# Kernel tuning notes

Hardware: AMD Instinct MI355X
Metric: run time of the kernel (lower is better)

Reference implementation:

```python
import jax, jax.numpy as jnp
import numpy as np

C, SHOT, D = 64, 16, 320
LN_EPS = 1e-5


def setup_inputs() -> dict:
    key = jax.random.key(0)
    ks = jax.random.split(key, 20)
    s = 0.05
    inp = {
        "input_x_mean": jax.random.normal(ks[0], (C, D), jnp.float32),
        "input_x": jax.random.normal(ks[1], (C * SHOT, D), jnp.float32),
        # embedding_same / embedding_diff Linear(D, D)
        "W_same": jax.random.normal(ks[2], (D, D), jnp.float32) * s,
        "b_same": jnp.zeros((D,), jnp.float32),
        "W_diff": jax.random.normal(ks[3], (D, D), jnp.float32) * s,
        "b_diff": jnp.zeros((D,), jnp.float32),
        # 1-head MultiHeadAttention(d_model=d_k=d_v=D)
        "Wq": jax.random.normal(ks[4], (D, D), jnp.float32) * s,
        "bq": jnp.zeros((D,), jnp.float32),
        "Wk": jax.random.normal(ks[5], (D, D), jnp.float32) * s,
        "bk": jnp.zeros((D,), jnp.float32),
        "Wv": jax.random.normal(ks[6], (D, D), jnp.float32) * s,
        "bv": jnp.zeros((D,), jnp.float32),
        "Wfc": jax.random.normal(ks[7], (D, D), jnp.float32) * s,
        "bfc": jnp.zeros((D,), jnp.float32),
        "ln_g": jnp.ones((D,), jnp.float32),
        "ln_b": jnp.zeros((D,), jnp.float32),
        # output Linear(D, 1)
        "Wout": jax.random.normal(ks[8], (D, 1), jnp.float32) * s,
        "bout": jnp.zeros((1,), jnp.float32),
    }
    return inp


def _mha(q, k, v, Wq, bq, Wk, bk, Wv, bv, Wfc, bfc, ln_g, ln_b):
    # Standard 1-head attention: proj -> scaled softmax attn -> fc -> residual + LayerNorm
    residual = q
    temp = jnp.sqrt(jnp.asarray(q.shape[-1], q.dtype))
    qp = q @ Wq + bq
    kp = k @ Wk + bk
    vp = v @ Wv + bv
    attn = jax.nn.softmax(jnp.einsum('bld,bmd->blm', qp, kp) / temp, axis=-1)
    out = jnp.einsum('blm,bmd->bld', attn, vp)
    out = out @ Wfc + bfc
    out = out + residual
    mu = out.mean(-1, keepdims=True)
    var = ((out - mu) ** 2).mean(-1, keepdims=True)
    return ln_g * (out - mu) * jax.lax.rsqrt(var + LN_EPS) + ln_b


def reference(input_x_mean, input_x, W_same, b_same, W_diff, b_diff,
              Wq, bq, Wk, bk, Wv, bv, Wfc, bfc, ln_g, ln_b, Wout, bout):
    c, d = input_x_mean.shape
    shot = input_x.shape[0] // c
    x = input_x.reshape(c, shot, d)

    # ---- Difference_Estimator ----
    same_diff = x - input_x_mean[:, None, :]                     # (C, shot, D)
    cls = np.arange(c)
    other = np.stack([np.concatenate([cls[:i], cls[i + 1:]]) for i in range(c)])  # (C, C-1)
    idx = (other[:, :, None] * shot + np.arange(shot)[None, None, :]).reshape(c, (c - 1) * shot)
    diff_diff = input_x_mean[:, None, :] - input_x[idx]          # (C, (C-1)*shot, D)

    # ---- Mean_Aggregator (one odefunc evaluation; state = input_x_mean) ----
    ps = (same_diff @ W_same + b_same) - input_x_mean[:, None, :]
    pd = (diff_diff @ W_diff + b_diff) - input_x_mean[:, None, :]
    ts = _mha(ps, ps, ps, Wq, bq, Wk, bk, Wv, bv, Wfc, bfc, ln_g, ln_b)
    td = _mha(pd, pd, pd, Wq, bq, Wk, bk, Wv, bv, Wfc, bfc, ln_g, ln_b)
    sm_s = jax.nn.softmax(ts @ Wout + bout, axis=1)              # (C, shot, 1)
    sm_d = jax.nn.softmax(td @ Wout + bout, axis=1)              # (C, (C-1)*shot, 1)
    weighted = jnp.concatenate([sm_s * ps, sm_d * pd], axis=1)   # (C, C*shot, D)
    return weighted.mean(axis=1)                                 # (C, D)
```

## Files before the change

kernel.cpp:

```cpp
#include <hip/hip_runtime.h>

#define CC   64
#define SHOT 16
#define DD   320
#define ND   1008
#define MS   (CC * SHOT)
#define MD   (CC * ND)
#define MT   (MD + MS)
#define LN_EPS 1e-5f

typedef __attribute__((ext_vector_type(8)))  short short8;
typedef __attribute__((ext_vector_type(4)))  float floatx4;
typedef __attribute__((ext_vector_type(4)))  int i32x4;

__device__ __forceinline__ unsigned short f2b(float f) {
  union { float f; unsigned int u; } v; v.f = f;
  unsigned int r = v.u + 0x7FFFu + ((v.u >> 16) & 1u);
  return (unsigned short)(r >> 16);
}
__device__ __forceinline__ float b2f(unsigned short b) {
  union { unsigned int u; float f; } v; v.u = ((unsigned int)b) << 16; return v.f;
}
__device__ __forceinline__ unsigned int pk2(float a, float b) {
  return (unsigned int)f2b(a) | ((unsigned int)f2b(b) << 16);
}
__device__ __forceinline__ void gl_lds16(const void* g, void* l) {
  __builtin_amdgcn_global_load_lds(
      (const __attribute__((address_space(1))) unsigned int*)g,
      (__attribute__((address_space(3))) unsigned int*)l, 16, 0, 0);
}
__device__ __forceinline__ floatx4 mfma16(short8 a, short8 b, floatx4 c) {
  return __builtin_amdgcn_mfma_f32_16x16x32_bf16(a, b, c, 0, 0, 0);
}
#define BARRIER_VM()  do { asm volatile("s_waitcnt vmcnt(0) lgkmcnt(0)" ::: "memory"); \
                           __builtin_amdgcn_s_barrier(); \
                           __builtin_amdgcn_sched_barrier(0); } while (0)

__global__ __launch_bounds__(256, 2) void gemm_mfma(
    const unsigned short* __restrict__ A,
    const float* __restrict__ Xg, const float* __restrict__ Xmean,
    const int mode,
    const unsigned short* __restrict__ BtDiff,
    const unsigned short* __restrict__ BtSame,
    const float* __restrict__ biasDiff, const float* __restrict__ biasSame,
    unsigned short* __restrict__ OutB,
    const unsigned short* __restrict__ ResB)
{
  __shared__ __align__(16) unsigned short As[2][128 * 64];
  __shared__ __align__(16) unsigned short Bs[2][64 * 64];
  const int t  = threadIdx.x;
  const int m0 = blockIdx.x * 128;
  const int n0 = blockIdx.y * 64;
  const int wid = t >> 6, lane = t & 63;
  const int wm = wid >> 1, wn = wid & 1;
  const int l15 = lane & 15, lg = lane >> 4;

  const bool isDiff = (m0 < MD);
  const unsigned short* Bt = (mode == 3 && !isDiff) ? BtSame : BtDiff;
  const float* bias = (mode == 3 && !isDiff) ? biasSame : biasDiff;

  const int ra = t >> 1, kh = t & 1;
  const float* aptr = nullptr; const float* mptr = nullptr;
  float sa = 1.f;
  if (mode == 3) {
    const int am = m0 + ra;
    if (isDiff) {
      const int c = am / ND, j = am - c * ND;
      const int oi = j >> 4, s = j & 15;
      const int oc = (oi < c) ? oi : oi + 1;
      aptr = Xg + (size_t)(oc * SHOT + s) * DD;
      mptr = Xmean + (size_t)c * DD;
      sa = -1.f;
    } else {
      const int ls = am - MD;
      aptr = Xg + (size_t)ls * DD;
      mptr = Xmean + (size_t)(ls >> 4) * DD;
      sa = 1.f;
    }
  }

  floatx4 acc[4][2];
  #pragma unroll
  for (int i = 0; i < 4; ++i)
    #pragma unroll
    for (int j = 0; j < 2; ++j) acc[i][j] = (floatx4){0.f, 0.f, 0.f, 0.f};

  auto stage = [&](int ks, int bufi) {
    const int k0 = ks * 64;
    #pragma unroll
    for (int it = 0; it < 2; ++it) {
      const int L = it * 256 + t;
      const int r = L >> 3, cs = L & 7;
      const int cl = cs ^ (r & 7);
      gl_lds16(Bt + (size_t)(n0 + r) * DD + k0 + cl * 8, &Bs[bufi][0] + L * 8);
    }
    if (mode == 0) {
      #pragma unroll
      for (int it = 0; it < 4; ++it) {
        const int L = it * 256 + t;
        const int r = L >> 3, cs = L & 7;
        const int cl = cs ^ (r & 7);
        gl_lds16(A + (size_t)(m0 + r) * DD + k0 + cl * 8, &As[bufi][0] + L * 8);
      }
    } else {
      const int kb2 = k0 + kh * 32;
      #pragma unroll
      for (int i = 0; i < 4; ++i) {
        const float4 x0  = *(const float4*)(aptr + kb2 + i * 8);
        const float4 x1  = *(const float4*)(aptr + kb2 + i * 8 + 4);
        const float4 mv0 = *(const float4*)(mptr + kb2 + i * 8);
        const float4 mv1 = *(const float4*)(mptr + kb2 + i * 8 + 4);
        i32x4 w;
        w[0] = (int)pk2(sa * (x0.x - mv0.x), sa * (x0.y - mv0.y));
        w[1] = (int)pk2(sa * (x0.z - mv0.z), sa * (x0.w - mv0.w));
        w[2] = (int)pk2(sa * (x1.x - mv1.x), sa * (x1.y - mv1.y));
        w[3] = (int)pk2(sa * (x1.z - mv1.z), sa * (x1.w - mv1.w));
        const int c  = kh * 4 + i;
        const int cw = c ^ (ra & 7);
        *(i32x4*)((char*)&As[bufi][0] + ra * 128 + cw * 16) = w;
      }
    }
  };

  auto compute = [&](int bufi) {
    #pragma unroll
    for (int kc = 0; kc < 2; ++kc) {
      short8 af[4], bf[2];
      #pragma unroll
      for (int mt = 0; mt < 4; ++mt) {
        const int row = wm * 64 + mt * 16 + l15;
        const int cs  = (kc * 4 + lg) ^ (row & 7);
        af[mt] = *(const short8*)((const char*)&As[bufi][0] + row * 128 + cs * 16);
      }
      #pragma unroll
      for (int nt = 0; nt < 2; ++nt) {
        const int row = wn * 32 + nt * 16 + l15;
        const int cs  = (kc * 4 + lg) ^ (row & 7);
        bf[nt] = *(const short8*)((const char*)&Bs[bufi][0] + row * 128 + cs * 16);
      }
      #pragma unroll
      for (int mt = 0; mt < 4; ++mt)
        #pragma unroll
        for (int nt = 0; nt < 2; ++nt)
          acc[mt][nt] = mfma16(af[mt], bf[nt], acc[mt][nt]);
    }
  };

  stage(0, 0);
  BARRIER_VM();
  for (int ks = 0; ks < 5; ++ks) {
    if (ks + 1 < 5) stage(ks + 1, (ks + 1) & 1);
    compute(ks & 1);
    BARRIER_VM();
  }

  #pragma unroll
  for (int nt = 0; nt < 2; ++nt) {
    const int n = n0 + wn * 32 + nt * 16 + l15;
    const float bb = bias[n];
    #pragma unroll
    for (int mt = 0; mt < 4; ++mt) {
      #pragma unroll
      for (int r = 0; r < 4; ++r) {
        const int m = m0 + wm * 64 + mt * 16 + lg * 4 + r;
        float v = acc[mt][nt][r] + bb;
        if (mode == 3) {
          const int cm = isDiff ? (m / ND) : ((m - MD) >> 4);
          v -= Xmean[(size_t)cm * DD + n];
        }
        if (ResB) v += b2f(ResB[(size_t)m * DD + n]);
        OutB[(size_t)m * DD + n] = f2b(v);
      }
    }
  }
}

__global__ __launch_bounds__(256, 2) void attn16(
    const unsigned short* __restrict__ Qg, const unsigned short* __restrict__ Pk,
    const unsigned short* __restrict__ Pt, unsigned short* __restrict__ Ob,
    const int qRows,
    const int kPitch,
    const int vtPitch,
    const int nKT, const int validKV, const int bpc, const int qTiles)
{
  __shared__ __align__(16) char smem[64 * 656];
  const int t = threadIdx.x;
  const int wid = t >> 6, lane = t & 63;
  const int l15 = lane & 15, lg = lane >> 4;

  int bx = blockIdx.x;
  const int nwg = gridDim.x;
  if ((nwg & 7) == 0) bx = (bx & 7) * (nwg >> 3) + (bx >> 3);
  const int cls  = bx / bpc;
  const int blkq = bx - cls * bpc;
  const int qt0 = blkq * 4 + wid;
  const bool wValid = qt0 < qTiles;
  const int qt = wValid ? qt0 : qTiles - 1;

  short8 qf[10];
  {
    const unsigned short* qrow = Qg + ((size_t)cls * qRows + qt * 16 + l15) * DD;
    #pragma unroll
    for (int kc = 0; kc < 10; ++kc) qf[kc] = *(const short8*)(qrow + kc * 32 + lg * 8);
  }

  floatx4 o[20];
  #pragma unroll
  for (int i = 0; i < 20; ++i) o[i] = (floatx4){0.f, 0.f, 0.f, 0.f};
  float mrun = -1e30f, lsum = 0.f;
  const float scale = 0.05590169943749474f;

  for (int kt = 0; kt < nKT; ++kt) {
    __syncthreads();
    #pragma unroll
    for (int it = 0; it < 5; ++it) {
      const int L = it * 256 + t;
      const int r = L / 40, c = L - (L / 40) * 40;
      const int cl = (c & ~7) | ((c & 7) ^ (r & 7));
      gl_lds16(Pk + ((size_t)cls * kPitch + kt * 32 + r) * DD + cl * 8, smem + L * 16);
    }
    #pragma unroll
    for (int it = 0; it < 5; ++it) {
      const int L = it * 256 + t;
      const int d = L >> 2, c = L & 3;
      const int cl = c ^ ((d >> 1) & 3);
      gl_lds16(Pt + ((size_t)cls * DD + d) * vtPitch + kt * 32 + cl * 8,
               smem + 20480 + L * 16);
    }
    __syncthreads();

    floatx4 st0 = (floatx4){0.f,0.f,0.f,0.f}, st1 = (floatx4){0.f,0.f,0.f,0.f};
    __builtin_amdgcn_s_setprio(1);
    #pragma unroll
    for (int kc = 0; kc < 10; ++kc) {
      const int c = kc * 4 + lg;
      const int cl = (c & ~7) | ((c & 7) ^ (l15 & 7));
      const short8 k0f = *(const short8*)(smem + l15 * 640 + cl * 16);
      const short8 k1f = *(const short8*)(smem + (16 + l15) * 640 + cl * 16);
      st0 = mfma16(k0f, qf[kc], st0);
      st1 = mfma16(k1f, qf[kc], st1);
    }
    __builtin_amdgcn_s_setprio(0);

    float s[8];
    #pragma unroll
    for (int r = 0; r < 4; ++r) { s[r] = st0[r] * scale; s[4 + r] = st1[r] * scale; }
    const int kvb = kt * 32 + lg * 4;
    #pragma unroll
    for (int r = 0; r < 4; ++r) {
      if (kvb + r      >= validKV) s[r]     = -1e30f;
      if (kvb + 16 + r >= validKV) s[4 + r] = -1e30f;
    }
    float mt_ = s[0];
    #pragma unroll
    for (int i = 1; i < 8; ++i) mt_ = fmaxf(mt_, s[i]);
    mt_ = fmaxf(mt_, __shfl_xor(mt_, 16));
    mt_ = fmaxf(mt_, __shfl_xor(mt_, 32));
    const float newm = fmaxf(mrun, mt_);
    if (__any(newm > mrun)) {
      const float alpha = __expf(mrun - newm);
      lsum *= alpha;
      #pragma unroll
      for (int i = 0; i < 20; ++i) {
        o[i][0] *= alpha; o[i][1] *= alpha; o[i][2] *= alpha; o[i][3] *= alpha;
      }
      mrun = newm;
    }
    float p[8]; float rs = 0.f;
    #pragma unroll
    for (int i = 0; i < 8; ++i) { p[i] = __expf(s[i] - mrun); rs += p[i]; }
    rs += __shfl_xor(rs, 16);
    rs += __shfl_xor(rs, 32);
    lsum += rs;

    const unsigned int pk00 = pk2(p[0], p[1]), pk01 = pk2(p[2], p[3]);
    const unsigned int pk10 = pk2(p[4], p[5]), pk11 = pk2(p[6], p[7]);
    const int src0 = l15 + ((lane >> 4) & 1) * 32;
    const int src1 = src0 + 16;
    const int y0 = __shfl((int)pk00, src0), y1 = __shfl((int)pk01, src0);
    const int y2 = __shfl((int)pk00, src1), y3 = __shfl((int)pk01, src1);
    const int z0 = __shfl((int)pk10, src0), z1 = __shfl((int)pk11, src0);
    const int z2 = __shfl((int)pk10, src1), z3 = __shfl((int)pk11, src1);
    const bool hi = lane >= 32;
    union { i32x4 w; short8 v; } pf;
    pf.w[0] = hi ? z0 : y0; pf.w[1] = hi ? z1 : y1;
    pf.w[2] = hi ? z2 : y2; pf.w[3] = hi ? z3 : y3;

    const int vswz = (l15 >> 1) & 3;
    __builtin_amdgcn_s_setprio(1);
    #pragma unroll
    for (int dt = 0; dt < 20; ++dt) {
      const int d = dt * 16 + l15;
      const short8 a = *(const short8*)(smem + 20480 + d * 64 + ((lg ^ vswz) << 4));
      o[dt] = mfma16(a, pf.v, o[dt]);
    }
    __builtin_amdgcn_s_setprio(0);
  }

  const float invl = 1.f / lsum;
  __syncthreads();
  char* ep = smem + wid * 10496;
  #pragma unroll
  for (int dt = 0; dt < 20; ++dt) {
    const unsigned int w0 = pk2(o[dt][0] * invl, o[dt][1] * invl);
    const unsigned int w1 = pk2(o[dt][2] * invl, o[dt][3] * invl);
    *(unsigned int*)(ep + l15 * 656 + (dt * 16 + lg * 4) * 2)     = w0;
    *(unsigned int*)(ep + l15 * 656 + (dt * 16 + lg * 4 + 2) * 2) = w1;
  }
  __syncthreads();
  if (wValid) {
    #pragma unroll
    for (int it = 0; it < 10; ++it) {
      const int flat = it * 64 + lane;
      const int q = flat / 40, c = flat - (flat / 40) * 40;
      const i32x4 v = *(const i32x4*)(ep + q * 656 + c * 16);
      *(i32x4*)(Ob + ((size_t)cls * qRows + qt * 16 + q) * DD + c * 8) = v;
    }
  }
}

__global__ __launch_bounds__(256) void transpose_p(
    const unsigned short* __restrict__ P, unsigned short* __restrict__ PtG,
    const int rowsP, const int vtPitch, const int kvTilesPerCls)
{
  __shared__ __align__(16) unsigned short Ls[64 * 72];
  const int t = threadIdx.x;
  const int cls = blockIdx.x / kvTilesPerCls;
  const int kvt = blockIdx.x - cls * kvTilesPerCls;
  const int dt = blockIdx.y;
  #pragma unroll
  for (int i = 0; i < 2; ++i) {
    const int flat = t + i * 256;
    const int r = flat >> 3, c = flat & 7;
    const int kv = kvt * 64 + r;
    i32x4 v = {0, 0, 0, 0};
    if (kv < rowsP)
      v = *(const i32x4*)(P + ((size_t)cls * rowsP + kv) * DD + dt * 64 + c * 8);
    *(i32x4*)(&Ls[r * 72 + c * 8]) = v;
  }
  __syncthreads();
  #pragma unroll
  for (int i = 0; i < 2; ++i) {
    const int flat = t + i * 256;
    const int r2 = flat >> 3, c2 = flat & 7;
    if (kvt * 64 + c2 * 8 < vtPitch) {
      union { unsigned short e[8]; i32x4 v; } u;
      #pragma unroll
      for (int jj = 0; jj < 8; ++jj) u.e[jj] = Ls[(c2 * 8 + jj) * 72 + r2];
      *(i32x4*)(PtG + ((size_t)cls * DD + dt * 64 + r2) * vtPitch + kvt * 64 + c2 * 8) = u.v;
    }
  }
}

__global__ __launch_bounds__(256) void wprep(
    const float* __restrict__ Wsame, const float* __restrict__ Wdiff,
    const float* __restrict__ Wk, const float* __restrict__ Wq,
    const float* __restrict__ Wfc, const float* __restrict__ Wv,
    unsigned short* __restrict__ BtS, unsigned short* __restrict__ BtD,
    unsigned short* __restrict__ BtG, unsigned short* __restrict__ BtVF)
{
  __shared__ float Ls[64 * 68];
  const int t = threadIdx.x;
  const int z = blockIdx.z;
  if (z < 2) {
    const float* W = z ? Wdiff : Wsame;
    unsigned short* Wt = z ? BtD : BtS;
    const int k0 = blockIdx.x * 64, n0 = blockIdx.y * 64;
    #pragma unroll
    for (int i = 0; i < 4; ++i) {
      const int flat = t + i * 256;
      const int r = flat >> 4, c = (flat & 15) * 4;
      *(float4*)&Ls[r * 68 + c] = *(const float4*)(W + (size_t)(k0 + r) * DD + n0 + c);
    }
    __syncthreads();
    #pragma unroll
    for (int j = 0; j < 2; ++j) {
      const int flat = t + j * 256;
      const int r2 = flat >> 3, c2 = flat & 7;
      union { unsigned short e[8]; i32x4 v; } u;
      #pragma unroll
      for (int jj = 0; jj < 8; ++jj) u.e[jj] = f2b(Ls[(c2 * 8 + jj) * 68 + r2]);
      *(i32x4*)(Wt + (size_t)(n0 + r2) * DD + k0 + c2 * 8) = u.v;
    }
  } else {
    const int trL = (z == 3);
    const float* L = trL ? Wfc : Wk;
    const float* R = trL ? Wv : Wq;
    unsigned short* Bt = trL ? BtVF : BtG;
    float* Lsm = Ls;
    float* Rsm = Ls + 16 * 68;
    const int n0 = blockIdx.x * 64, k0 = blockIdx.y * 64;
    const int tn4 = (t & 15) * 4, tk4 = (t >> 4) * 4;
    float acc[4][4] = {};
    for (int ms = 0; ms < DD; ms += 16) {
      const int lr = t >> 4, lc = (t & 15);
      #pragma unroll
      for (int i = 0; i < 4; ++i) {
        const int nn = lc * 4 + i;
        Lsm[lr * 68 + nn] = trL ? L[(size_t)(ms + lr) * DD + n0 + nn]
                                : L[(size_t)(n0 + nn) * DD + ms + lr];
        Rsm[lr * 68 + nn] = R[(size_t)(k0 + nn) * DD + ms + lr];
      }
      __syncthreads();
      #pragma unroll
      for (int mm = 0; mm < 16; ++mm) {
        float la[4], rb[4];
        #pragma unroll
        for (int i = 0; i < 4; ++i) { la[i] = Lsm[mm * 68 + tn4 + i]; rb[i] = Rsm[mm * 68 + tk4 + i]; }
        #pragma unroll
        for (int i = 0; i < 4; ++i)
          #pragma unroll
          for (int j = 0; j < 4; ++j) acc[i][j] += la[i] * rb[j];
      }
      __syncthreads();
    }
    #pragma unroll
    for (int i = 0; i < 4; ++i)
      #pragma unroll
      for (int j = 0; j < 4; ++j)
        Bt[(size_t)(n0 + tn4 + i) * DD + k0 + tk4 + j] = f2b(acc[i][j]);
  }
}

__global__ __launch_bounds__(640) void wbias(
    const float* __restrict__ Wk, const float* __restrict__ bq,
    const float* __restrict__ Wfc, const float* __restrict__ bv,
    const float* __restrict__ bfc, float* __restrict__ v, float* __restrict__ bvf)
{
  const int t = threadIdx.x;
  if (t < DD) {
    float a = 0.f;
    for (int m = 0; m < DD; ++m) a += Wk[(size_t)t * DD + m] * bq[m];
    v[t] = a;
  } else if (t < 2 * DD) {
    const int n = t - DD;
    float a = 0.f;
    for (int m = 0; m < DD; ++m) a += Wfc[(size_t)m * DD + n] * bv[m];
    bvf[n] = a + bfc[n];
  }
}

__global__ __launch_bounds__(256) void ln_logit(
    const unsigned short* __restrict__ X, const float* __restrict__ gam,
    const float* __restrict__ bet, const float* __restrict__ Wout,
    const float* __restrict__ bout, float* __restrict__ logits, const int M)
{
  const int row = blockIdx.x * 4 + (threadIdx.x >> 6);
  if (row >= M) return;
  const int lane = threadIdx.x & 63;
  const unsigned short* x = X + (size_t)row * DD;
  float v[5]; float s = 0.f;
  #pragma unroll
  for (int i = 0; i < 5; ++i) { v[i] = b2f(x[lane + 64 * i]); s += v[i]; }
  #pragma unroll
  for (int off = 32; off; off >>= 1) s += __shfl_xor(s, off);
  const float mu = s * (1.f / DD);
  float q = 0.f;
  #pragma unroll
  for (int i = 0; i < 5; ++i) { const float d = v[i] - mu; q += d * d; }
  #pragma unroll
  for (int off = 32; off; off >>= 1) q += __shfl_xor(q, off);
  const float inv = rsqrtf(q * (1.f / DD) + LN_EPS);
  float lg = 0.f;
  #pragma unroll
  for (int i = 0; i < 5; ++i) {
    const int k = lane + 64 * i;
    lg += (gam[k] * (v[i] - mu) * inv + bet[k]) * Wout[k];
  }
  #pragma unroll
  for (int off = 32; off; off >>= 1) lg += __shfl_xor(lg, off);
  if (lane == 0) logits[row] = lg + bout[0];
}

__global__ __launch_bounds__(320) void final_reduce(
    const float* __restrict__ logits_s, const float* __restrict__ logits_d,
    const unsigned short* __restrict__ Ps, const unsigned short* __restrict__ Pd,
    float* __restrict__ out)
{
  const int c = blockIdx.x;
  const int t = threadIdx.x;
  __shared__ float w[16 + ND];
  __shared__ float red[5];
  if (t < 16) w[t] = logits_s[c * 16 + t];
  for (int j = t; j < ND; j += 320) w[16 + j] = logits_d[c * ND + j];
  __syncthreads();
  if (t == 0) {
    float mx = w[0];
    #pragma unroll
    for (int i = 1; i < 16; ++i) mx = fmaxf(mx, w[i]);
    float ssum = 0.f;
    #pragma unroll
    for (int i = 0; i < 16; ++i) { const float e = __expf(w[i] - mx); w[i] = e; ssum += e; }
    const float inv = 1.f / ssum;
    #pragma unroll
    for (int i = 0; i < 16; ++i) w[i] *= inv;
  }
  float lm = -1e30f;
  for (int j = t; j < ND; j += 320) lm = fmaxf(lm, w[16 + j]);
  #pragma unroll
  for (int off = 32; off; off >>= 1) lm = fmaxf(lm, __shfl_xor(lm, off));
  if ((t & 63) == 0) red[t >> 6] = lm;
  __syncthreads();
  const float mx = fmaxf(fmaxf(fmaxf(red[0], red[1]), fmaxf(red[2], red[3])), red[4]);
  float ls = 0.f;
  for (int j = t; j < ND; j += 320) { const float e = __expf(w[16 + j] - mx); w[16 + j] = e; ls += e; }
  #pragma unroll
  for (int off = 32; off; off >>= 1) ls += __shfl_xor(ls, off);
  __syncthreads();
  if ((t & 63) == 0) red[t >> 6] = ls;
  __syncthreads();
  const float inv = 1.f / (red[0] + red[1] + red[2] + red[3] + red[4]);
  for (int j = t; j < ND; j += 320) w[16 + j] *= inv;
  __syncthreads();
  float acc = 0.f;
  const unsigned short* Psc = Ps + (size_t)c * SHOT * DD + t;
  const unsigned short* Pdc = Pd + (size_t)c * ND * DD + t;
  #pragma unroll 4
  for (int i = 0; i < 16; ++i) acc += w[i] * b2f(Psc[(size_t)i * DD]);
  for (int j = 0; j < ND; ++j) acc += w[16 + j] * b2f(Pdc[(size_t)j * DD]);
  out[c * DD + t] = acc * (1.f / 1024.f);
}

extern "C" void kernel_launch(void* const* d_in, const int* in_sizes, int n_in,
                              void* d_out, int out_size, void* d_ws, size_t ws_size,
                              hipStream_t stream)
{
  const float* xmean = (const float*)d_in[0];
  const float* x     = (const float*)d_in[1];
  const float* Wsame = (const float*)d_in[2];
  const float* bsame = (const float*)d_in[3];
  const float* Wdiff = (const float*)d_in[4];
  const float* bdiff = (const float*)d_in[5];
  const float* Wq    = (const float*)d_in[6];
  const float* bq    = (const float*)d_in[7];
  const float* Wk    = (const float*)d_in[8];
  const float* bk    = (const float*)d_in[9];   (void)bk;
  const float* Wv    = (const float*)d_in[10];
  const float* bv    = (const float*)d_in[11];
  const float* Wfc   = (const float*)d_in[12];
  const float* bfc   = (const float*)d_in[13];
  const float* lng   = (const float*)d_in[14];
  const float* lnb   = (const float*)d_in[15];
  const float* Wout  = (const float*)d_in[16];
  const float* boutp = (const float*)d_in[17];
  float* outp = (float*)d_out;

  char* base = (char*)d_ws;
  size_t off = 0;
  auto alloc = [&](size_t bytes) { char* p = base + off; off += (bytes + 255) & ~(size_t)255; return p; };

  const size_t WB = (size_t)DD * DD * 2;
  unsigned short* BtS  = (unsigned short*)alloc(WB);
  unsigned short* BtD  = (unsigned short*)alloc(WB);
  unsigned short* BtG  = (unsigned short*)alloc(WB);
  unsigned short* BtVF = (unsigned short*)alloc(WB);
  float* vbias = (float*)alloc(DD * 4);
  float* bvf   = (float*)alloc(DD * 4);
  unsigned short* P_b  = (unsigned short*)alloc((size_t)MT * DD * 2);
  unsigned short* Qg_b = (unsigned short*)alloc((size_t)MT * DD * 2);
  unsigned short* O_b  = (unsigned short*)alloc((size_t)MT * DD * 2);
  unsigned short* PtD  = (unsigned short*)alloc((size_t)CC * DD * 1024 * 2);
  unsigned short* PtS  = (unsigned short*)alloc((size_t)CC * DD * 32 * 2);
  float* logits = (float*)alloc((size_t)MT * 4);

  const dim3 blk(256);
  wprep<<<dim3(5, 5, 4), blk, 0, stream>>>(Wsame, Wdiff, Wk, Wq, Wfc, Wv,
                                           BtS, BtD, BtG, BtVF);
  wbias<<<dim3(1), dim3(640), 0, stream>>>(Wk, bq, Wfc, bv, bfc, vbias, bvf);

  const dim3 gAll(MT / 128, 5);
  gemm_mfma<<<gAll, blk, 0, stream>>>(nullptr, x, xmean, 3, BtD, BtS,
                                      bdiff, bsame, P_b, nullptr);
  transpose_p<<<dim3(CC * 16, 5), blk, 0, stream>>>(P_b, PtD, ND, 1024, 16);
  transpose_p<<<dim3(CC, 5), blk, 0, stream>>>(P_b + (size_t)MD * DD, PtS, 16, 32, 1);
  gemm_mfma<<<gAll, blk, 0, stream>>>(P_b, nullptr, nullptr, 0, BtG, nullptr,
                                      vbias, nullptr, Qg_b, nullptr);
  attn16<<<dim3(CC * 16), blk, 0, stream>>>(Qg_b, P_b, PtD, O_b,
                                            ND, ND, 1024, 32, ND, 16, 63);
  attn16<<<dim3(CC), blk, 0, stream>>>(Qg_b + (size_t)MD * DD, P_b + (size_t)MD * DD,
                                       PtS, O_b + (size_t)MD * DD,
                                       16, 16, 32, 1, 16, 1, 1);
  gemm_mfma<<<gAll, blk, 0, stream>>>(O_b, nullptr, nullptr, 0, BtVF, nullptr,
                                      bvf, nullptr, Qg_b, P_b);
  ln_logit<<<dim3(MT / 4), blk, 0, stream>>>(Qg_b, lng, lnb, Wout, boutp, logits, MT);
  final_reduce<<<dim3(CC), dim3(320), 0, stream>>>(logits + MD, logits,
                                                   P_b + (size_t)MD * DD, P_b, outp);
}
```

Measured before the change: 488.2 us.

## Fold Q·K weight product into P GEMM, fuse LayerNorm-logit into FC epilogue

The Q·Wk-style projection is precomposed with the embedding weights (Wdiff/Wsame) and the mean term, so one z-split GEMM writes both P and Qg straight from the fp32 inputs instead of a second GEMM reading P. The FC GEMM epilogue now produces per-row partial sums (sum, sum of squares, u·x), and LayerNorm plus the output projection collapse into a tiny logits kernel, removing the bf16 write and reread of the FC output. The diff and same attention launches and transposes are merged, and online-softmax rescaling is skipped unless the max grows by more than 8. Risks include extra weight-prep work, lower precision from composing weights, and E[x²]−mu² variance cancellation.

```diff
diff --git a/kernel.cpp b/kernel.cpp
--- a/kernel.cpp
+++ b/kernel.cpp
@@ -36,33 +36,35 @@
                            __builtin_amdgcn_s_barrier(); \
                            __builtin_amdgcn_sched_barrier(0); } while (0)
 
-__global__ __launch_bounds__(256, 2) void gemm_mfma(
-    const unsigned short* __restrict__ A,
+__global__ __launch_bounds__(256, 2) void gemm_p_qg(
     const float* __restrict__ Xg, const float* __restrict__ Xmean,
-    const int mode,
-    const unsigned short* __restrict__ BtDiff,
-    const unsigned short* __restrict__ BtSame,
-    const float* __restrict__ biasDiff, const float* __restrict__ biasSame,
-    unsigned short* __restrict__ OutB,
-    const unsigned short* __restrict__ ResB)
+    const unsigned short* __restrict__ BtD, const unsigned short* __restrict__ BtS,
+    const unsigned short* __restrict__ BtDG, const unsigned short* __restrict__ BtSG,
+    const float* __restrict__ bdiff, const float* __restrict__ bsame,
+    const float* __restrict__ bqg, const float* __restrict__ bsg,
+    const float* __restrict__ Mg,
+    unsigned short* __restrict__ P_b, unsigned short* __restrict__ Qg_b)
 {
   __shared__ __align__(16) unsigned short As[2][128 * 64];
   __shared__ __align__(16) unsigned short Bs[2][64 * 64];
   const int t  = threadIdx.x;
   const int m0 = blockIdx.x * 128;
   const int n0 = blockIdx.y * 64;
+  const int z  = blockIdx.z;
   const int wid = t >> 6, lane = t & 63;
   const int wm = wid >> 1, wn = wid & 1;
   const int l15 = lane & 15, lg = lane >> 4;
 
   const bool isDiff = (m0 < MD);
-  const unsigned short* Bt = (mode == 3 && !isDiff) ? BtSame : BtDiff;
-  const float* bias = (mode == 3 && !isDiff) ? biasSame : biasDiff;
+  const unsigned short* Bt = z ? (isDiff ? BtDG : BtSG) : (isDiff ? BtD : BtS);
+  const float* bias = z ? (isDiff ? bqg : bsg) : (isDiff ? bdiff : bsame);
+  const float* mean = z ? Mg : Xmean;
+  unsigned short* OutB = z ? Qg_b : P_b;
 
   const int ra = t >> 1, kh = t & 1;
-  const float* aptr = nullptr; const float* mptr = nullptr;
-  float sa = 1.f;
-  if (mode == 3) {
+  const float* aptr; const float* mptr;
+  float sa;
+  {
     const int am = m0 + ra;
     if (isDiff) {
       const int c = am / ND, j = am - c * ND;
@@ -94,31 +96,21 @@
       const int cl = cs ^ (r & 7);
       gl_lds16(Bt + (size_t)(n0 + r) * DD + k0 + cl * 8, &Bs[bufi][0] + L * 8);
     }
-    if (mode == 0) {
-      #pragma unroll
-      for (int it = 0; it < 4; ++it) {
-        const int L = it * 256 + t;
-        const int r = L >> 3, cs = L & 7;
-        const int cl = cs ^ (r & 7);
-        gl_lds16(A + (size_t)(m0 + r) * DD + k0 + cl * 8, &As[bufi][0] + L * 8);
-      }
-    } else {
-      const int kb2 = k0 + kh * 32;
-      #pragma unroll
-      for (int i = 0; i < 4; ++i) {
-        const float4 x0  = *(const float4*)(aptr + kb2 + i * 8);
-        const float4 x1  = *(const float4*)(aptr + kb2 + i * 8 + 4);
-        const float4 mv0 = *(const float4*)(mptr + kb2 + i * 8);
-        const float4 mv1 = *(const float4*)(mptr + kb2 + i * 8 + 4);
-        i32x4 w;
-        w[0] = (int)pk2(sa * (x0.x - mv0.x), sa * (x0.y - mv0.y));
-        w[1] = (int)pk2(sa * (x0.z - mv0.z), sa * (x0.w - mv0.w));
-        w[2] = (int)pk2(sa * (x1.x - mv1.x), sa * (x1.y - mv1.y));
-        w[3] = (int)pk2(sa * (x1.z - mv1.z), sa * (x1.w - mv1.w));
-        const int c  = kh * 4 + i;
-        const int cw = c ^ (ra & 7);
-        *(i32x4*)((char*)&As[bufi][0] + ra * 128 + cw * 16) = w;
-      }
+    const int kb2 = k0 + kh * 32;
+    #pragma unroll
+    for (int i = 0; i < 4; ++i) {
+      const float4 x0  = *(const float4*)(aptr + kb2 + i * 8);
+      const float4 x1  = *(const float4*)(aptr + kb2 + i * 8 + 4);
+      const float4 mv0 = *(const float4*)(mptr + kb2 + i * 8);
+      const float4 mv1 = *(const float4*)(mptr + kb2 + i * 8 + 4);
+      i32x4 w;
+      w[0] = (int)pk2(sa * (x0.x - mv0.x), sa * (x0.y - mv0.y));
+      w[1] = (int)pk2(sa * (x0.z - mv0.z), sa * (x0.w - mv0.w));
+      w[2] = (int)pk2(sa * (x1.x - mv1.x), sa * (x1.y - mv1.y));
+      w[3] = (int)pk2(sa * (x1.z - mv1.z), sa * (x1.w - mv1.w));
+      const int c  = kh * 4 + i;
+      const int cw = c ^ (ra & 7);
+      *(i32x4*)((char*)&As[bufi][0] + ra * 128 + cw * 16) = w;
     }
   };
 
@@ -163,25 +155,124 @@
       #pragma unroll
       for (int r = 0; r < 4; ++r) {
         const int m = m0 + wm * 64 + mt * 16 + lg * 4 + r;
-        float v = acc[mt][nt][r] + bb;
-        if (mode == 3) {
-          const int cm = isDiff ? (m / ND) : ((m - MD) >> 4);
-          v -= Xmean[(size_t)cm * DD + n];
-        }
-        if (ResB) v += b2f(ResB[(size_t)m * DD + n]);
+        const int cm = isDiff ? (m / ND) : ((m - MD) >> 4);
+        const float v = acc[mt][nt][r] + bb - mean[(size_t)cm * DD + n];
         OutB[(size_t)m * DD + n] = f2b(v);
       }
     }
   }
 }
 
+__global__ __launch_bounds__(256, 2) void gemm_fc(
+    const unsigned short* __restrict__ A,
+    const unsigned short* __restrict__ Bt,
+    const float* __restrict__ bvf,
+    const unsigned short* __restrict__ ResB,
+    const float* __restrict__ u,
+    float* __restrict__ part)
+{
+  __shared__ __align__(16) unsigned short As[2][128 * 64];
+  __shared__ __align__(16) unsigned short Bs[2][64 * 64];
+  const int t  = threadIdx.x;
+  const int m0 = blockIdx.x * 128;
+  const int n0 = blockIdx.y * 64;
+  const int wid = t >> 6, lane = t & 63;
+  const int wm = wid >> 1, wn = wid & 1;
+  const int l15 = lane & 15, lg = lane >> 4;
+
+  floatx4 acc[4][2];
+  #pragma unroll
+  for (int i = 0; i < 4; ++i)
+    #pragma unroll
+    for (int j = 0; j < 2; ++j) acc[i][j] = (floatx4){0.f, 0.f, 0.f, 0.f};
+
+  auto stage = [&](int ks, int bufi) {
+    const int k0 = ks * 64;
+    #pragma unroll
+    for (int it = 0; it < 2; ++it) {
+      const int L = it * 256 + t;
+      const int r = L >> 3, cs = L & 7;
+      const int cl = cs ^ (r & 7);
+      gl_lds16(Bt + (size_t)(n0 + r) * DD + k0 + cl * 8, &Bs[bufi][0] + L * 8);
+    }
+    #pragma unroll
+    for (int it = 0; it < 4; ++it) {
+      const int L = it * 256 + t;
+      const int r = L >> 3, cs = L & 7;
+      const int cl = cs ^ (r & 7);
+      gl_lds16(A + (size_t)(m0 + r) * DD + k0 + cl * 8, &As[bufi][0] + L * 8);
+    }
+  };
+
+  auto compute = [&](int bufi) {
+    #pragma unroll
+    for (int kc = 0; kc < 2; ++kc) {
+      short8 af[4], bf[2];
+      #pragma unroll
+      for (int mt = 0; mt < 4; ++mt) {
+        const int row = wm * 64 + mt * 16 + l15;
+        const int cs  = (kc * 4 + lg) ^ (row & 7);
+        af[mt] = *(const short8*)((const char*)&As[bufi][0] + row * 128 + cs * 16);
+      }
+      #pragma unroll
+      for (int nt = 0; nt < 2; ++nt) {
+        const int row = wn * 32 + nt * 16 + l15;
+        const int cs  = (kc * 4 + lg) ^ (row & 7);
+        bf[nt] = *(const short8*)((const char*)&Bs[bufi][0] + row * 128 + cs * 16);
+      }
+      #pragma unroll
+      for (int mt = 0; mt < 4; ++mt)
+        #pragma unroll
+        for (int nt = 0; nt < 2; ++nt)
+          acc[mt][nt] = mfma16(af[mt], bf[nt], acc[mt][nt]);
+    }
+  };
+
+  stage(0, 0);
+  BARRIER_VM();
+  for (int ks = 0; ks < 5; ++ks) {
+    if (ks + 1 < 5) stage(ks + 1, (ks + 1) & 1);
+    compute(ks & 1);
+    BARRIER_VM();
+  }
+
+  const int slot = blockIdx.y * 2 + wn;
+  #pragma unroll
+  for (int mt = 0; mt < 4; ++mt) {
+    float ps0[4] = {0.f,0.f,0.f,0.f}, ps1[4] = {0.f,0.f,0.f,0.f}, ps2[4] = {0.f,0.f,0.f,0.f};
+    #pragma unroll
+    for (int nt = 0; nt < 2; ++nt) {
+      const int n = n0 + wn * 32 + nt * 16 + l15;
+      const float bb = bvf[n];
+      const float un = u[n];
+      #pragma unroll
+      for (int r = 0; r < 4; ++r) {
+        const int m = m0 + wm * 64 + mt * 16 + lg * 4 + r;
+        const float v = acc[mt][nt][r] + bb + b2f(ResB[(size_t)m * DD + n]);
+        ps0[r] += v; ps1[r] += v * v; ps2[r] += un * v;
+      }
+    }
+    #pragma unroll
+    for (int r = 0; r < 4; ++r) {
+      #pragma unroll
+      for (int mk = 1; mk < 16; mk <<= 1) {
+        ps0[r] += __shfl_xor(ps0[r], mk);
+        ps1[r] += __shfl_xor(ps1[r], mk);
+        ps2[r] += __shfl_xor(ps2[r], mk);
+      }
+      if (l15 == 0) {
+        const int m = m0 + wm * 64 + mt * 16 + lg * 4 + r;
+        float* pp = part + ((size_t)m * 10 + slot) * 3;
+        pp[0] = ps0[r]; pp[1] = ps1[r]; pp[2] = ps2[r];
+      }
+    }
+  }
+}
+
 __global__ __launch_bounds__(256, 2) void attn16(
-    const unsigned short* __restrict__ Qg, const unsigned short* __restrict__ Pk,
-    const unsigned short* __restrict__ Pt, unsigned short* __restrict__ Ob,
-    const int qRows,
-    const int kPitch,
-    const int vtPitch,
-    const int nKT, const int validKV, const int bpc, const int qTiles)
+    const unsigned short* __restrict__ Qall, const unsigned short* __restrict__ Pall,
+    const unsigned short* __restrict__ PtD, const unsigned short* __restrict__ PtS,
+    unsigned short* __restrict__ Oall)
 {
   __shared__ __align__(16) char smem[64 * 656];
   const int t = threadIdx.x;
@@ -190,9 +281,20 @@
 
   int bx = blockIdx.x;
   const int nwg = gridDim.x;
-  if ((nwg & 7) == 0) bx = (bx & 7) * (nwg >> 3) + (bx >> 3);
-  const int cls  = bx / bpc;
-  const int blkq = bx - cls * bpc;
+  bx = (bx & 7) * (nwg >> 3) + (bx >> 3);
+
+  const unsigned short *Qg, *Pk, *Pt; unsigned short* Ob;
+  int cls, blkq, qRows, kPitch, vtPitch, nKT, validKV, qTiles;
+  if (bx < 1024) {
+    cls = bx >> 4; blkq = bx & 15;
+    Qg = Qall; Pk = Pall; Pt = PtD; Ob = Oall;
+    qRows = ND; kPitch = ND; vtPitch = 1024; nKT = 32; validKV = ND; qTiles = 63;
+  } else {
+    cls = bx - 1024; blkq = 0;
+    Qg = Qall + (size_t)MD * DD; Pk = Pall + (size_t)MD * DD;
+    Pt = PtS; Ob = Oall + (size_t)MD * DD;
+    qRows = 16; kPitch = 16; vtPitch = 32; nKT = 1; validKV = 16; qTiles = 1;
+  }
   const int qt0 = blkq * 4 + wid;
   const bool wValid = qt0 < qTiles;
   const int qt = wValid ? qt0 : qTiles - 1;
@@ -256,8 +358,8 @@
     for (int i = 1; i < 8; ++i) mt_ = fmaxf(mt_, s[i]);
     mt_ = fmaxf(mt_, __shfl_xor(mt_, 16));
     mt_ = fmaxf(mt_, __shfl_xor(mt_, 32));
-    const float newm = fmaxf(mrun, mt_);
-    if (__any(newm > mrun)) {
+    if (!__all(mt_ - mrun <= 8.0f)) {
+      const float newm = fmaxf(mrun, mt_);
       const float alpha = __expf(mrun - newm);
       lsum *= alpha;
       #pragma unroll
@@ -319,14 +421,19 @@
   }
 }
 
-__global__ __launch_bounds__(256) void transpose_p(
-    const unsigned short* __restrict__ P, unsigned short* __restrict__ PtG,
-    const int rowsP, const int vtPitch, const int kvTilesPerCls)
+__global__ __launch_bounds__(256) void transpose_pm(
+    const unsigned short* __restrict__ Pall,
+    unsigned short* __restrict__ PtD, unsigned short* __restrict__ PtS)
 {
   __shared__ __align__(16) unsigned short Ls[64 * 72];
   const int t = threadIdx.x;
-  const int cls = blockIdx.x / kvTilesPerCls;
-  const int kvt = blockIdx.x - cls * kvTilesPerCls;
+  const int bx = blockIdx.x;
+  const unsigned short* P; unsigned short* PtG;
+  int cls, kvt, rowsP, vtPitch;
+  if (bx < 1024) { cls = bx >> 4; kvt = bx & 15; P = Pall; PtG = PtD;
+                   rowsP = ND; vtPitch = 1024; }
+  else { cls = bx - 1024; kvt = 0; P = Pall + (size_t)MD * DD; PtG = PtS;
+         rowsP = 16; vtPitch = 32; }
   const int dt = blockIdx.y;
   #pragma unroll
   for (int i = 0; i < 2; ++i) {
@@ -357,7 +464,7 @@
     const float* __restrict__ Wk, const float* __restrict__ Wq,
     const float* __restrict__ Wfc, const float* __restrict__ Wv,
     unsigned short* __restrict__ BtS, unsigned short* __restrict__ BtD,
-    unsigned short* __restrict__ BtG, unsigned short* __restrict__ BtVF)
+    float* __restrict__ GfT, unsigned short* __restrict__ BtVF)
 {
   __shared__ float Ls[64 * 68];
   const int t = threadIdx.x;
@@ -386,7 +493,6 @@
     const int trL = (z == 3);
     const float* L = trL ? Wfc : Wk;
     const float* R = trL ? Wv : Wq;
-    unsigned short* Bt = trL ? BtVF : BtG;
     float* Lsm = Ls;
     float* Rsm = Ls + 16 * 68;
     const int n0 = blockIdx.x * 64, k0 = blockIdx.y * 64;
@@ -414,18 +520,103 @@
       }
       __syncthreads();
     }
+    if (z == 2) {
+      #pragma unroll
+      for (int i = 0; i < 4; ++i)
+        #pragma unroll
+        for (int j = 0; j < 4; ++j)
+          GfT[(size_t)(n0 + tn4 + i) * DD + k0 + tk4 + j] = acc[i][j];
+    } else {
+      #pragma unroll
+      for (int i = 0; i < 4; ++i)
+        #pragma unroll
+        for (int j = 0; j < 4; ++j)
+          BtVF[(size_t)(n0 + tn4 + i) * DD + k0 + tk4 + j] = f2b(acc[i][j]);
+    }
+  }
+}
+
+__global__ __launch_bounds__(256) void wprep2(
+    const float* __restrict__ GfT,
+    const float* __restrict__ Wdiff, const float* __restrict__ Wsame,
+    const float* __restrict__ Xmean,
+    const float* __restrict__ bdiff, const float* __restrict__ bsame,
+    const float* __restrict__ vbias,
+    unsigned short* __restrict__ BtDG, unsigned short* __restrict__ BtSG,
+    float* __restrict__ Mg, float* __restrict__ bqg, float* __restrict__ bsg)
+{
+  __shared__ float Ls[2 * 16 * 68];
+  const int t = threadIdx.x;
+  const int z = blockIdx.z;
+  if (z < 2) {
+    const float* R = z ? Wsame : Wdiff;
+    unsigned short* Bt = z ? BtSG : BtDG;
+    float* Lsm = Ls;
+    float* Rsm = Ls + 16 * 68;
+    const int n0 = blockIdx.x * 64, k0 = blockIdx.y * 64;
+    const int tn4 = (t & 15) * 4, tk4 = (t >> 4) * 4;
+    float acc[4][4] = {};
+    for (int ms = 0; ms < DD; ms += 16) {
+      const int lr = t >> 4, lc = (t & 15);
+      #pragma unroll
+      for (int i = 0; i < 4; ++i) {
+        const int nn = lc * 4 + i;
+        Lsm[lr * 68 + nn] = GfT[(size_t)(n0 + nn) * DD + ms + lr];
+        Rsm[lr * 68 + nn] = R[(size_t)(k0 + nn) * DD + ms + lr];
+      }
+      __syncthreads();
+      #pragma unroll
+      for (int mm = 0; mm < 16; ++mm) {
+        float la[4], rb[4];
+        #pragma unroll
+        for (int i = 0; i < 4; ++i) { la[i] = Lsm[mm * 68 + tn4 + i]; rb[i] = Rsm[mm * 68 + tk4 + i]; }
+        #pragma unroll
+        for (int i = 0; i < 4; ++i)
+          #pragma unroll
+          for (int j = 0; j < 4; ++j) acc[i][j] += la[i] * rb[j];
+      }
+      __syncthreads();
+    }
     #pragma unroll
     for (int i = 0; i < 4; ++i)
       #pragma unroll
       for (int j = 0; j < 4; ++j)
         Bt[(size_t)(n0 + tn4 + i) * DD + k0 + tk4 + j] = f2b(acc[i][j]);
-  }
-}
-
-__global__ __launch_bounds__(640) void wbias(
+  } else {
+    const int n0 = blockIdx.y * 64;
+    if (blockIdx.x == 0) {
+      for (int idx = t; idx < 64 * 64; idx += 256) {
+        const int c = idx >> 6, nn = n0 + (idx & 63);
+        float a = 0.f;
+        for (int k = 0; k < DD; ++k) a += Xmean[c * DD + k] * GfT[(size_t)nn * DD + k];
+        Mg[c * DD + nn] = a;
+      }
+    } else if (blockIdx.x == 1) {
+      if (t < 64) {
+        const int nn = n0 + t;
+        float a = 0.f;
+        for (int k = 0; k < DD; ++k) a += bdiff[k] * GfT[(size_t)nn * DD + k];
+        bqg[nn] = a + vbias[nn];
+      }
+    } else if (blockIdx.x == 2) {
+      if (t < 64) {
+        const int nn = n0 + t;
+        float a = 0.f;
+        for (int k = 0; k < DD; ++k) a += bsame[k] * GfT[(size_t)nn * DD + k];
+        bsg[nn] = a + vbias[nn];
+      }
+    }
+  }
+}
+
+__global__ __launch_bounds__(960) void wbias(
     const float* __restrict__ Wk, const float* __restrict__ bq,
     const float* __restrict__ Wfc, const float* __restrict__ bv,
-    const float* __restrict__ bfc, float* __restrict__ v, float* __restrict__ bvf)
+    const float* __restrict__ bfc,
+    const float* __restrict__ lng, const float* __restrict__ lnb,
+    const float* __restrict__ Wout, const float* __restrict__ bout,
+    float* __restrict__ v, float* __restrict__ bvf,
+    float* __restrict__ u, float* __restrict__ scal)
 {
   const int t = threadIdx.x;
   if (t < DD) {
@@ -437,39 +628,30 @@
     float a = 0.f;
     for (int m = 0; m < DD; ++m) a += Wfc[(size_t)m * DD + n] * bv[m];
     bvf[n] = a + bfc[n];
-  }
-}
-
-__global__ __launch_bounds__(256) void ln_logit(
-    const unsigned short* __restrict__ X, const float* __restrict__ gam,
-    const float* __restrict__ bet, const float* __restrict__ Wout,
-    const float* __restrict__ bout, float* __restrict__ logits, const int M)
-{
-  const int row = blockIdx.x * 4 + (threadIdx.x >> 6);
-  if (row >= M) return;
-  const int lane = threadIdx.x & 63;
-  const unsigned short* x = X + (size_t)row * DD;
-  float v[5]; float s = 0.f;
-  #pragma unroll
-  for (int i = 0; i < 5; ++i) { v[i] = b2f(x[lane + 64 * i]); s += v[i]; }
-  #pragma unroll
-  for (int off = 32; off; off >>= 1) s += __shfl_xor(s, off);
-  const float mu = s * (1.f / DD);
-  float q = 0.f;
-  #pragma unroll
-  for (int i = 0; i < 5; ++i) { const float d = v[i] - mu; q += d * d; }
-  #pragma unroll
-  for (int off = 32; off; off >>= 1) q += __shfl_xor(q, off);
-  const float inv = rsqrtf(q * (1.f / DD) + LN_EPS);
-  float lg = 0.f;
-  #pragma unroll
-  for (int i = 0; i < 5; ++i) {
-    const int k = lane + 64 * i;
-    lg += (gam[k] * (v[i] - mu) * inv + bet[k]) * Wout[k];
-  }
-  #pragma unroll
-  for (int off = 32; off; off >>= 1) lg += __shfl_xor(lg, off);
-  if (lane == 0) logits[row] = lg + bout[0];
+  } else if (t < 3 * DD) {
+    const int n = t - 2 * DD;
+    u[n] = lng[n] * Wout[n];
+    if (n == 0) {
+      float su = 0.f, b0 = 0.f;
+      for (int k = 0; k < DD; ++k) { su += lng[k] * Wout[k]; b0 += lnb[k] * Wout[k]; }
+      scal[0] = su; scal[1] = b0 + bout[0];
+    }
+  }
+}
+
+__global__ __launch_bounds__(256) void logits_k(
+    const float* __restrict__ part, const float* __restrict__ scal,
+    float* __restrict__ logits)
+{
+  const int m = blockIdx.x * 256 + threadIdx.x;
+  const float* pp = part + (size_t)m * 30;
+  float sF = 0.f, sF2 = 0.f, sUF = 0.f;
+  #pragma unroll
+  for (int s = 0; s < 10; ++s) { sF += pp[s * 3]; sF2 += pp[s * 3 + 1]; sUF += pp[s * 3 + 2]; }
+  const float mu  = sF * (1.f / DD);
+  const float var = sF2 * (1.f / DD) - mu * mu;
+  const float inv = rsqrtf(var + LN_EPS);
+  logits[m] = inv * (sUF - mu * scal[0]) + scal[1];
 }
 
 __global__ __launch_bounds__(320) void final_reduce(
@@ -552,37 +734,38 @@
   const size_t WB = (size_t)DD * DD * 2;
   unsigned short* BtS  = (unsigned short*)alloc(WB);
   unsigned short* BtD  = (unsigned short*)alloc(WB);
-  unsigned short* BtG  = (unsigned short*)alloc(WB);
+  unsigned short* BtDG = (unsigned short*)alloc(WB);
+  unsigned short* BtSG = (unsigned short*)alloc(WB);
   unsigned short* BtVF = (unsigned short*)alloc(WB);
+  float* GfT   = (float*)alloc((size_t)DD * DD * 4);
+  float* Mg    = (float*)alloc((size_t)CC * DD * 4);
   float* vbias = (float*)alloc(DD * 4);
   float* bvf   = (float*)alloc(DD * 4);
+  float* bqg   = (float*)alloc(DD * 4);
+  float* bsg   = (float*)alloc(DD * 4);
+  float* ubuf  = (float*)alloc(DD * 4);
+  float* scal  = (float*)alloc(2 * 4);
   unsigned short* P_b  = (unsigned short*)alloc((size_t)MT * DD * 2);
   unsigned short* Qg_b = (unsigned short*)alloc((size_t)MT * DD * 2);
   unsigned short* O_b  = (unsigned short*)alloc((size_t)MT * DD * 2);
   unsigned short* PtD  = (unsigned short*)alloc((size_t)CC * DD * 1024 * 2);
   unsigned short* PtS  = (unsigned short*)alloc((size_t)CC * DD * 32 * 2);
+  float* part   = (float*)alloc((size_t)MT * 30 * 4);
   float* logits = (float*)alloc((size_t)MT * 4);
 
   const dim3 blk(256);
   wprep<<<dim3(5, 5, 4), blk, 0, stream>>>(Wsame, Wdiff, Wk, Wq, Wfc, Wv,
-                                           BtS, BtD, BtG, BtVF);
-  wbias<<<dim3(1), dim3(640), 0, stream>>>(Wk, bq, Wfc, bv, bfc, vbias, bvf);
-
-  const dim3 gAll(MT / 128, 5);
-  gemm_mfma<<<gAll, blk, 0, stream>>>(nullptr, x, xmean, 3, BtD, BtS,
-                                      bdiff, bsame, P_b, nullptr);
-  transpose_p<<<dim3(CC * 16, 5), blk, 0, stream>>>(P_b, PtD, ND, 1024, 16);
-  transpose_p<<<dim3(CC, 5), blk, 0, stream>>>(P_b + (size_t)MD * DD, PtS, 16, 32, 1);
-  gemm_mfma<<<gAll, blk, 0, stream>>>(P_b, nullptr, nullptr, 0, BtG, nullptr,
-                                      vbias, nullptr, Qg_b, nullptr);
-  attn16<<<dim3(CC * 16), blk, 0, stream>>>(Qg_b, P_b, PtD, O_b,
-                                            ND, ND, 1024, 32, ND, 16, 63);
-  attn16<<<dim3(CC), blk, 0, stream>>>(Qg_b + (size_t)MD * DD, P_b + (size_t)MD * DD,
-                                       PtS, O_b + (size_t)MD * DD,
-                                       16, 16, 32, 1, 16, 1, 1);
-  gemm_mfma<<<gAll, blk, 0, stream>>>(O_b, nullptr, nullptr, 0, BtVF, nullptr,
-                                      bvf, nullptr, Qg_b, P_b);
-  ln_logit<<<dim3(MT / 4), blk, 0, stream>>>(Qg_b, lng, lnb, Wout, boutp, logits, MT);
+                                           BtS, BtD, GfT, BtVF);
+  wbias<<<dim3(1), dim3(960), 0, stream>>>(Wk, bq, Wfc, bv, bfc, lng, lnb, Wout, boutp,
+                                           vbias, bvf, ubuf, scal);
+  wprep2<<<dim3(5, 5, 3), blk, 0, stream>>>(GfT, Wdiff, Wsame, xmean, bdiff, bsame,
+                                            vbias, BtDG, BtSG, Mg, bqg, bsg);
+  gemm_p_qg<<<dim3(MT / 128, 5, 2), blk, 0, stream>>>(
+      x, xmean, BtD, BtS, BtDG, BtSG, bdiff, bsame, bqg, bsg, Mg, P_b, Qg_b);
+  transpose_pm<<<dim3(1088, 5), blk, 0, stream>>>(P_b, PtD, PtS);
+  attn16<<<dim3(1088), blk, 0, stream>>>(Qg_b, P_b, PtD, PtS, O_b);
+  gemm_fc<<<dim3(MT / 128, 5), blk, 0, stream>>>(O_b, BtVF, bvf, P_b, ubuf, part);
+  logits_k<<<dim3(MT / 256), blk, 0, stream>>>(part, scal, logits);
   final_reduce<<<dim3(CC), dim3(320), 0, stream>>>(logits + MD, logits,
                                                    P_b + (size_t)MD * DD, P_b, outp);
 }
```

Measured after the change: 699.6 us. 1.43x slower.
